# Optimization experiments

Hardware: AMD Instinct MI355X
Metric: run time of the kernel (lower is better)

The kernel has to match this reference:

```python
import jax, jax.numpy as jnp
import numpy as np

DIM = 256
NUM_HEADS = 8
HEAD_DIM = DIM // NUM_HEADS
CPB_HIDDEN = 512
B, N = 2, 2304
TABLE = 9025  # (2*48-1)**2


def _l2norm(t, eps=1e-12):
    # matches torch F.normalize(dim=-1): x / max(||x||, eps)
    n = jnp.sqrt(jnp.sum(t * t, axis=-1, keepdims=True))
    return t / jnp.maximum(n, eps)


def setup_inputs() -> dict:
    key = jax.random.key(0)
    ks = jax.random.split(key, 12)
    x = jax.random.normal(ks[0], (B, N, DIM), dtype=jnp.float32)
    relative_pos_index = jax.random.randint(ks[1], (N, N), 0, TABLE, dtype=jnp.int64)
    relative_coords_table = jax.random.uniform(ks[2], (TABLE, 2), dtype=jnp.float32) * 2.0 - 1.0
    seq_length_scale = jnp.ones((1,), dtype=jnp.float32) * jnp.log2(jnp.float32(N))
    padding_mask = jnp.zeros((B, N), dtype=jnp.int32)
    s = 0.02
    W_qkv = jax.random.normal(ks[3], (3 * DIM, DIM), dtype=jnp.float32) * s
    b_qkv = jnp.zeros((3 * DIM,), dtype=jnp.float32)
    # temperature init: log(exp(1/0.24) - 1) so softplus(temperature) = 1/0.24
    temperature = jnp.full((NUM_HEADS, 1, 1), float(np.log(np.expm1(1.0 / 0.24))), dtype=jnp.float32)
    query_embedding = jax.random.normal(ks[4], (NUM_HEADS, 1, HEAD_DIM), dtype=jnp.float32) * s
    W_proj = jax.random.normal(ks[5], (DIM, DIM), dtype=jnp.float32) * s
    b_proj = jnp.zeros((DIM,), dtype=jnp.float32)
    W_cpb1 = jax.random.normal(ks[6], (CPB_HIDDEN, 2), dtype=jnp.float32) * s
    b_cpb1 = jnp.zeros((CPB_HIDDEN,), dtype=jnp.float32)
    W_cpb2 = jax.random.normal(ks[7], (NUM_HEADS, CPB_HIDDEN), dtype=jnp.float32) * s
    b_cpb2 = jnp.zeros((NUM_HEADS,), dtype=jnp.float32)
    return {
        'x': x, 'relative_pos_index': relative_pos_index,
        'relative_coords_table': relative_coords_table,
        'seq_length_scale': seq_length_scale, 'padding_mask': padding_mask,
        'W_qkv': W_qkv, 'b_qkv': b_qkv, 'temperature': temperature,
        'query_embedding': query_embedding, 'W_proj': W_proj, 'b_proj': b_proj,
        'W_cpb1': W_cpb1, 'b_cpb1': b_cpb1, 'W_cpb2': W_cpb2, 'b_cpb2': b_cpb2,
    }


def reference(x, relative_pos_index, relative_coords_table, seq_length_scale,
              padding_mask, W_qkv, b_qkv, temperature, query_embedding,
              W_proj, b_proj, W_cpb1, b_cpb1, W_cpb2, b_cpb2):
    Bx, Nx, C = x.shape
    h, d = NUM_HEADS, HEAD_DIM
    # qkv projection -> (B, 3h, N, d); first h heads = q, then k, then v
    qkv = (jnp.einsum('bnc,oc->bno', x, W_qkv) + b_qkv)
    qkv = qkv.reshape(Bx, Nx, 3 * h, d).transpose(0, 2, 1, 3)
    q, k, v = qkv[:, :h], qkv[:, h:2 * h], qkv[:, 2 * h:]
    # CPB relative bias: (T,2) -> (T,h) -> (h,N,N) via gather
    hid = jax.nn.relu(relative_coords_table @ W_cpb1.T + b_cpb1)
    tab = hid @ W_cpb2.T + b_cpb2                    # (T, h)
    rel_bias = tab.T[:, relative_pos_index.reshape(-1)].reshape(h, Nx, Nx)
    # cosine-sim attention with learned query embedding + softplus temperature
    scale = jax.nn.softplus(temperature) * seq_length_scale[0]   # (h,1,1)
    qn = (_l2norm(q) + query_embedding) * scale                  # (B,h,N,d)
    kn = _l2norm(k)
    attn = jnp.einsum('bhnd,bhmd->bhnm', qn, kn) + rel_bias
    attn = jax.nn.softmax(attn, axis=-1)
    out = jnp.einsum('bhnm,bhmd->bhnd', attn, v)
    out = out.transpose(0, 2, 1, 3).reshape(Bx, Nx, C)
    out = out @ W_proj.T + b_proj
    return out
```

## Files before the change

kernel.cpp:

```cpp
#include <hip/hip_runtime.h>
#include <math.h>

#define DIMC 256
#define NHEADS 8
#define HDIM 32
#define CPBH 512
#define BB 2
#define NSEQ 2304
#define TAB 9025
#define TABP 9040
#define RTOT (BB*NHEADS*NSEQ)
#define SPLITS 4
#define MSP (NSEQ/SPLITS)
#define PBS 36
#define NCHUNK (NSEQ/32)
#define LOG2E 1.44269504088896340736f

#define NX  (BB*NSEQ*DIMC)
#define NWQ (3*DIMC*DIMC)
#define NWP (DIMC*DIMC)

#define SPLITX4_BLOCKS ((NX + NWQ + NWP) / 1024)
#define IDXP_ELEMS     (NSEQ * NCHUNK * 16)
#define IDXP4_BLOCKS   (IDXP_ELEMS / 1024)
#define CPB_BLOCKS     ((TAB + 63) / 64)

typedef unsigned short ushort;
typedef __attribute__((ext_vector_type(8))) short short8;
typedef __attribute__((ext_vector_type(4))) short short4v;
typedef __attribute__((ext_vector_type(4))) float f32x4;

#define MFMA16(a,b,c) __builtin_amdgcn_mfma_f32_16x16x32_bf16((a),(b),(c),0,0,0)

__device__ __forceinline__ ushort f2bf(float x) {
  unsigned u = __float_as_uint(x);
  u += 0x7FFFu + ((u >> 16) & 1u);
  return (ushort)(u >> 16);
}
__device__ __forceinline__ float bf2f(ushort b) {
  return __uint_as_float(((unsigned)b) << 16);
}
__device__ __forceinline__ float fexp2(float x) {
#if defined(__has_builtin)
#if __has_builtin(__builtin_amdgcn_exp2f)
  return __builtin_amdgcn_exp2f(x);
#else
  return exp2f(x);
#endif
#else
  return exp2f(x);
#endif
}
__device__ __forceinline__ unsigned pack_trunc(float p0, float p1) {
  return __builtin_amdgcn_perm(__float_as_uint(p1), __float_as_uint(p0), 0x07060302u);
}

__global__ void setup_kernel(const float* __restrict__ x, const float* __restrict__ wq,
                             const float* __restrict__ wp, const int* __restrict__ idx,
                             const float* __restrict__ tbl, const float* __restrict__ W1,
                             const float* __restrict__ b1, const float* __restrict__ W2,
                             const float* __restrict__ b2,
                             ushort* __restrict__ xh, ushort* __restrict__ xl,
                             ushort* __restrict__ wqh, ushort* __restrict__ wql,
                             ushort* __restrict__ wph, ushort* __restrict__ wpl,
                             unsigned* __restrict__ idxP, ushort* __restrict__ tabBf) {
  __shared__ float w1b[CPBH * 4];
  __shared__ float w2t[CPBH * NHEADS];
  __shared__ float part[4][64][NHEADS];
  int blk = blockIdx.x;
  int tid = threadIdx.x;
  if (blk < CPB_BLOCKS) {
    for (int i = tid; i < CPBH; i += 256) {
      w1b[i * 4 + 0] = W1[2 * i];
      w1b[i * 4 + 1] = W1[2 * i + 1];
      w1b[i * 4 + 2] = b1[i];
      w1b[i * 4 + 3] = 0.f;
    }
    for (int i = tid; i < CPBH * NHEADS; i += 256)
      w2t[(i & (CPBH - 1)) * NHEADS + (i >> 9)] = W2[i];
    int tl = tid & 63, jc = tid >> 6;
    int t = blk * 64 + tl;
    bool valid = t < TAB;
    float c0 = 0.f, c1 = 0.f;
    if (valid) { c0 = tbl[2 * t]; c1 = tbl[2 * t + 1]; }
    __syncthreads();
    float acc[NHEADS];
#pragma unroll
    for (int h = 0; h < NHEADS; ++h) acc[h] = 0.f;
    for (int j = jc * 128; j < jc * 128 + 128; ++j) {
      float4 wv = *(const float4*)&w1b[j * 4];
      float hid = fmaxf(fmaf(c0, wv.x, fmaf(c1, wv.y, wv.z)), 0.f);
      float4 wa = *(const float4*)&w2t[j * NHEADS];
      float4 wb = *(const float4*)&w2t[j * NHEADS + 4];
      acc[0] = fmaf(hid, wa.x, acc[0]);
      acc[1] = fmaf(hid, wa.y, acc[1]);
      acc[2] = fmaf(hid, wa.z, acc[2]);
      acc[3] = fmaf(hid, wa.w, acc[3]);
      acc[4] = fmaf(hid, wb.x, acc[4]);
      acc[5] = fmaf(hid, wb.y, acc[5]);
      acc[6] = fmaf(hid, wb.z, acc[6]);
      acc[7] = fmaf(hid, wb.w, acc[7]);
    }
#pragma unroll
    for (int h = 0; h < NHEADS; ++h) part[jc][tl][h] = acc[h];
    __syncthreads();
    if (jc == 0 && valid) {
#pragma unroll
      for (int h = 0; h < NHEADS; ++h) {
        float s = part[0][tl][h] + part[1][tl][h] + part[2][tl][h] + part[3][tl][h] + b2[h];
        tabBf[h * TABP + t] = f2bf(s * LOG2E);
      }
    }
  } else if (blk < CPB_BLOCKS + SPLITX4_BLOCKS) {
    int i = ((blk - CPB_BLOCKS) * 256 + tid) * 4;
    const float* src; ushort *hi, *lo; int j;
    if (i < NX)            { src = x;  hi = xh;  lo = xl;  j = i; }
    else if (i < NX + NWQ) { src = wq; hi = wqh; lo = wql; j = i - NX; }
    else                   { src = wp; hi = wph; lo = wpl; j = i - NX - NWQ; }
    float4 v = *(const float4*)&src[j];
    ushort h0 = f2bf(v.x), h1 = f2bf(v.y), h2 = f2bf(v.z), h3 = f2bf(v.w);
    uint2 hp, lp;
    hp.x = (unsigned)h0 | ((unsigned)h1 << 16);
    hp.y = (unsigned)h2 | ((unsigned)h3 << 16);
    lp.x = (unsigned)f2bf(v.x - bf2f(h0)) | ((unsigned)f2bf(v.y - bf2f(h1)) << 16);
    lp.y = (unsigned)f2bf(v.z - bf2f(h2)) | ((unsigned)f2bf(v.w - bf2f(h3)) << 16);
    *(uint2*)&hi[j] = hp;
    *(uint2*)&lo[j] = lp;
  } else {
    int t4 = (blk - CPB_BLOCKS - SPLITX4_BLOCKS) * 256 + tid;
    int cc4 = (t4 & 3) * 4;
    int ch = (t4 >> 2) % NCHUNK;
    int n = t4 / (4 * NCHUNK);
    int mbase = ch * 32 + cc4;
    int4 a = *(const int4*)&idx[(size_t)n * NSEQ + mbase];
    int4 b = *(const int4*)&idx[(size_t)n * NSEQ + mbase + 16];
    uint4 o;
    o.x = (unsigned)a.x | ((unsigned)b.x << 16);
    o.y = (unsigned)a.y | ((unsigned)b.y << 16);
    o.z = (unsigned)a.z | ((unsigned)b.z << 16);
    o.w = (unsigned)a.w | ((unsigned)b.w << 16);
    *(uint4*)&idxP[((size_t)n * NCHUNK + ch) * 16 + cc4] = o;
  }
}

__launch_bounds__(256)
__global__ void gemm_qkv(const ushort* __restrict__ Ah, const ushort* __restrict__ Al,
                         const ushort* __restrict__ Bh, const ushort* __restrict__ Bl,
                         const float* __restrict__ bias, const float* __restrict__ temp,
                         const float* __restrict__ sls, const float* __restrict__ qe,
                         ushort* __restrict__ qhi, ushort* __restrict__ qlo,
                         ushort* __restrict__ khi, ushort* __restrict__ klo,
                         ushort* __restrict__ vT) {
  __shared__ float vbuf[64][65];
  int tid = threadIdx.x;
  int lane = tid & 63, w = tid >> 6;
  int g = lane >> 4, c = lane & 15;
  int n0 = blockIdx.x * 64, m0 = blockIdx.y * 64;
  int mw = m0 + w * 16;
  const int K = DIMC;
  f32x4 acc[4] = {{0,0,0,0},{0,0,0,0},{0,0,0,0},{0,0,0,0}};
#pragma unroll 2
  for (int k0 = 0; k0 < K; k0 += 32) {
    short8 ah = *(const short8*)&Ah[(size_t)(mw + c) * K + k0 + g * 8];
    short8 al = *(const short8*)&Al[(size_t)(mw + c) * K + k0 + g * 8];
#pragma unroll
    for (int nt = 0; nt < 4; ++nt) {
      short8 bh = *(const short8*)&Bh[(size_t)(n0 + nt * 16 + c) * K + k0 + g * 8];
      short8 bl = *(const short8*)&Bl[(size_t)(n0 + nt * 16 + c) * K + k0 + g * 8];
      acc[nt] = MFMA16(ah, bh, acc[nt]);
      acc[nt] = MFMA16(al, bh, acc[nt]);
      acc[nt] = MFMA16(ah, bl, acc[nt]);
    }
  }
#pragma unroll
  for (int nt = 0; nt < 4; ++nt) {
    float bv = bias[n0 + nt * 16 + c];
#pragma unroll
    for (int r = 0; r < 4; ++r) acc[nt][r] += bv;
  }

  int b = (m0 >= NSEQ) ? 1 : 0;
  int nb = m0 - b * NSEQ;
  int sect = n0 >> 8;

  if (sect < 2) {
    int hloc = (n0 & 255) >> 5;
#pragma unroll
    for (int H = 0; H < 2; ++H) {
      int head = hloc + H;
      float scale = log1pf(expf(temp[head])) * sls[0] * LOG2E;
#pragma unroll
      for (int r = 0; r < 4; ++r) {
        float ss = acc[2*H][r]*acc[2*H][r] + acc[2*H+1][r]*acc[2*H+1][r];
        ss += __shfl_xor(ss, 1);
        ss += __shfl_xor(ss, 2);
        ss += __shfl_xor(ss, 4);
        ss += __shfl_xor(ss, 8);
        float inv = 1.f / fmaxf(sqrtf(ss), 1e-12f);
        int n = nb + w * 16 + g * 4 + r;
        size_t orow = ((size_t)(b * NHEADS + head) * NSEQ + n) * HDIM;
#pragma unroll
        for (int half = 0; half < 2; ++half) {
          int nt = 2*H + half;
          int d = half * 16 + c;
          float val = acc[nt][r] * inv;
          if (sect == 0) {
            val = (val + qe[head * HDIM + d]) * scale;
            ushort hh = f2bf(val);
            qhi[orow + d] = hh;
            qlo[orow + d] = f2bf(val - bf2f(hh));
          } else {
            ushort hh = f2bf(val);
            khi[orow + d] = hh;
            klo[orow + d] = f2bf(val - bf2f(hh));
          }
        }
      }
    }
  } else {
#pragma unroll
    for (int nt = 0; nt < 4; ++nt)
#pragma unroll
      for (int r = 0; r < 4; ++r)
        vbuf[w * 16 + g * 4 + r][nt * 16 + c] = acc[nt][r];
    __syncthreads();
    int hbase = (n0 - 512) >> 5;
#pragma unroll
    for (int it = 0; it < 16; ++it) {
      int dloc = (tid >> 6) * 16 + it;
      int p = tid & 63;
      int pp = p & 31;
      int nsrc = (p & 32) + (pp & 1) * 16 + (pp >> 1);
      float v = vbuf[nsrc][dloc];
      int head = hbase + (dloc >> 5), d = dloc & 31;
      vT[((size_t)((b * NHEADS + head) * HDIM + d)) * NSEQ + nb + p] = f2bf(v);
    }
  }
}

__launch_bounds__(256)
__global__ void attn_kernel(const ushort* __restrict__ qhi, const ushort* __restrict__ qlo,
                            const ushort* __restrict__ khi, const ushort* __restrict__ klo,
                            const ushort* __restrict__ vT, const ushort* __restrict__ tabBf,
                            const unsigned* __restrict__ idxP,
                            float* __restrict__ pO, float* __restrict__ pL) {
  __shared__ ushort tbf[10240];
  __shared__ __align__(16) ushort pbuf[8][16 * PBS];
  int tid = threadIdx.x;
  int lane = tid & 63;
  int w = tid >> 6;
  int qb = blockIdx.x;
  int by = blockIdx.y;
  int s = by & 3, bh = by >> 2;
  int h = bh & (NHEADS - 1);

  const ushort* tsrc = tabBf + h * TABP;
#pragma unroll
  for (int i = 0; i < 5; ++i) {
    int off = i * 2048 + tid * 8;
    *(int4*)&tbf[off] = *(const int4*)&tsrc[off];
  }

  int g = lane >> 4, c = lane & 15;
  int q0 = qb * 128 + w * 16;
  int q1 = q0 + 64;
  size_t rowbase = (size_t)bh * NSEQ;

  short8 qAh = *(const short8*)&qhi[(rowbase + q0 + c) * HDIM + g * 8];
  short8 qAl = *(const short8*)&qlo[(rowbase + q0 + c) * HDIM + g * 8];
  short8 qBh = *(const short8*)&qhi[(rowbase + q1 + c) * HDIM + g * 8];
  short8 qBl = *(const short8*)&qlo[(rowbase + q1 + c) * HDIM + g * 8];
  __syncthreads();

  short one = (c == 0) ? (short)0x3F80 : (short)0;
  short8 onesB = {one, one, one, one, one, one, one, one};

  f32x4 oa0 = {0,0,0,0}, oa1 = {0,0,0,0}, ob0 = {0,0,0,0}, ob1 = {0,0,0,0};
  f32x4 la = {0,0,0,0}, lb = {0,0,0,0};
  ushort* pba = pbuf[w * 2];
  ushort* pbb = pbuf[w * 2 + 1];
  int m0 = s * MSP;

#define LOADK(MT, D0H, D0L, D1H, D1L, IA0, IA1, IA2, IA3, IB0, IB1, IB2, IB3) do { \
    size_t ra_ = (rowbase + (MT) + c) * HDIM + g * 8;                 \
    D0H = *(const short8*)&khi[ra_];                                  \
    D0L = *(const short8*)&klo[ra_];                                  \
    D1H = *(const short8*)&khi[ra_ + 16 * HDIM];                      \
    D1L = *(const short8*)&klo[ra_ + 16 * HDIM];                      \
    size_t ia_ = ((size_t)(q0 + g * 4) * NCHUNK + ((MT) >> 5)) * 16 + c; \
    IA0 = idxP[ia_];                                                  \
    IA1 = idxP[ia_ + (size_t)NCHUNK * 16];                            \
    IA2 = idxP[ia_ + (size_t)2 * NCHUNK * 16];                        \
    IA3 = idxP[ia_ + (size_t)3 * NCHUNK * 16];                        \
    size_t ibx_ = ((size_t)(q1 + g * 4) * NCHUNK + ((MT) >> 5)) * 16 + c; \
    IB0 = idxP[ibx_];                                                 \
    IB1 = idxP[ibx_ + (size_t)NCHUNK * 16];                           \
    IB2 = idxP[ibx_ + (size_t)2 * NCHUNK * 16];                       \
    IB3 = idxP[ibx_ + (size_t)3 * NCHUNK * 16];                       \
  } while (0)

  short8 c0h, c0l, c1h, c1l;
  unsigned ia0, ia1, ia2, ia3, ib0, ib1, ib2, ib3;
  LOADK(m0, c0h, c0l, c1h, c1l, ia0, ia1, ia2, ia3, ib0, ib1, ib2, ib3);

  for (int mt = m0; mt < m0 + MSP; mt += 32) {
    int mtn = (mt + 32 < m0 + MSP) ? (mt + 32) : m0;
    short8 n0h, n0l, n1h, n1l;
    unsigned ja0, ja1, ja2, ja3, jb0, jb1, jb2, jb3;
    LOADK(mtn, n0h, n0l, n1h, n1l, ja0, ja1, ja2, ja3, jb0, jb1, jb2, jb3);

    f32x4 sa0 = {0,0,0,0}, sa1 = {0,0,0,0}, sb0 = {0,0,0,0}, sb1 = {0,0,0,0};
    sa0 = MFMA16(qAh, c0h, sa0);
    sb0 = MFMA16(qBh, c0h, sb0);
    sa1 = MFMA16(qAh, c1h, sa1);
    sb1 = MFMA16(qBh, c1h, sb1);
    sa0 = MFMA16(qAl, c0h, sa0);
    sb0 = MFMA16(qBl, c0h, sb0);
    sa1 = MFMA16(qAl, c1h, sa1);
    sb1 = MFMA16(qBl, c1h, sb1);
    sa0 = MFMA16(qAh, c0l, sa0);
    sb0 = MFMA16(qBh, c0l, sb0);
    sa1 = MFMA16(qAh, c1l, sa1);
    sb1 = MFMA16(qBh, c1l, sb1);

    size_t va = ((size_t)(bh * HDIM + c)) * NSEQ + mt + g * 8;
    short8 vf0 = *(const short8*)&vT[va];
    short8 vf1 = *(const short8*)&vT[va + 16 * NSEQ];

    unsigned ipa[4] = {ia0, ia1, ia2, ia3};
    unsigned ipb[4] = {ib0, ib1, ib2, ib3};
#pragma unroll
    for (int r = 0; r < 4; ++r) {
      int k0 = ipa[r] & 0xFFFF, k1 = ipa[r] >> 16;
      float pA0 = fexp2(sa0[r] + bf2f(tbf[k0]));
      float pA1 = fexp2(sa1[r] + bf2f(tbf[k1]));
      *(unsigned*)&pba[(g * 4 + r) * PBS + 2 * c] = pack_trunc(pA0, pA1);
    }
#pragma unroll
    for (int r = 0; r < 4; ++r) {
      int k0 = ipb[r] & 0xFFFF, k1 = ipb[r] >> 16;
      float pB0 = fexp2(sb0[r] + bf2f(tbf[k0]));
      float pB1 = fexp2(sb1[r] + bf2f(tbf[k1]));
      *(unsigned*)&pbb[(g * 4 + r) * PBS + 2 * c] = pack_trunc(pB0, pB1);
    }

    short4v paA = *(const short4v*)&pba[c * PBS + g * 8];
    short4v paB = *(const short4v*)&pba[c * PBS + g * 8 + 4];
    short8 pfa = __builtin_shufflevector(paA, paB, 0, 1, 2, 3, 4, 5, 6, 7);
    short4v pbA = *(const short4v*)&pbb[c * PBS + g * 8];
    short4v pbB = *(const short4v*)&pbb[c * PBS + g * 8 + 4];
    short8 pfb = __builtin_shufflevector(pbA, pbB, 0, 1, 2, 3, 4, 5, 6, 7);

    oa0 = MFMA16(pfa, vf0, oa0);
    oa1 = MFMA16(pfa, vf1, oa1);
    ob0 = MFMA16(pfb, vf0, ob0);
    ob1 = MFMA16(pfb, vf1, ob1);
    la  = MFMA16(pfa, onesB, la);
    lb  = MFMA16(pfb, onesB, lb);

    c0h = n0h; c0l = n0l; c1h = n1h; c1l = n1l;
    ia0 = ja0; ia1 = ja1; ia2 = ja2; ia3 = ja3;
    ib0 = jb0; ib1 = jb1; ib2 = jb2; ib3 = jb3;
  }
#undef LOADK

  size_t prow0 = (size_t)s * RTOT + rowbase;
#pragma unroll
  for (int r = 0; r < 4; ++r) {
    size_t pra = prow0 + q0 + g * 4 + r;
    pO[pra * HDIM + c]      = oa0[r];
    pO[pra * HDIM + 16 + c] = oa1[r];
    size_t prb = prow0 + q1 + g * 4 + r;
    pO[prb * HDIM + c]      = ob0[r];
    pO[prb * HDIM + 16 + c] = ob1[r];
    if (c == 0) { pL[pra] = la[r]; pL[prb] = lb[r]; }
  }
}

#define ALD 264
__launch_bounds__(256)
__global__ void gemm_proj_fused(const float* __restrict__ pO, const float* __restrict__ pL,
                                const ushort* __restrict__ Bh_, const ushort* __restrict__ Bl_,
                                const float* __restrict__ bias, float* __restrict__ C) {
  __shared__ __align__(16) ushort Ahs[64 * ALD];
  __shared__ __align__(16) ushort Als[64 * ALD];
  int tid = threadIdx.x;
  int m0 = blockIdx.x * 64;
  int b = (m0 >= NSEQ) ? 1 : 0;
  int nb = m0 - b * NSEQ;

  {
    int r = tid >> 2;
    int q = tid & 3;
    int n = nb + r;
#pragma unroll
    for (int h = 0; h < NHEADS; ++h) {
      size_t bhn = (size_t)(b * NHEADS + h) * NSEQ + n;
      float L = 0.f;
#pragma unroll
      for (int sp = 0; sp < SPLITS; ++sp) L += pL[(size_t)sp * RTOT + bhn];
      float inv = 1.f / L;
      float a[8] = {0.f, 0.f, 0.f, 0.f, 0.f, 0.f, 0.f, 0.f};
#pragma unroll
      for (int sp = 0; sp < SPLITS; ++sp) {
        const float* src = &pO[((size_t)sp * RTOT + bhn) * HDIM + q * 8];
        float4 v0 = *(const float4*)&src[0];
        float4 v1 = *(const float4*)&src[4];
        a[0] += v0.x; a[1] += v0.y; a[2] += v0.z; a[3] += v0.w;
        a[4] += v1.x; a[5] += v1.y; a[6] += v1.z; a[7] += v1.w;
      }
      ushort hi8[8], lo8[8];
#pragma unroll
      for (int i = 0; i < 8; ++i) {
        float v = a[i] * inv;
        ushort hh = f2bf(v);
        hi8[i] = hh;
        lo8[i] = f2bf(v - bf2f(hh));
      }
      int k = h * 32 + q * 8;
      *(int4*)&Ahs[r * ALD + k] = *(int4*)hi8;
      *(int4*)&Als[r * ALD + k] = *(int4*)lo8;
    }
  }
  __syncthreads();

  int lane = tid & 63, w = tid >> 6;
  int g = lane >> 4, c = lane & 15;
  int n0 = w * 64;
  f32x4 acc[4][4] = {};
  for (int k0 = 0; k0 < DIMC; k0 += 32) {
    short8 bfh[4], bfl[4];
#pragma unroll
    for (int nt = 0; nt < 4; ++nt) {
      bfh[nt] = *(const short8*)&Bh_[(size_t)(n0 + nt * 16 + c) * DIMC + k0 + g * 8];
      bfl[nt] = *(const short8*)&Bl_[(size_t)(n0 + nt * 16 + c) * DIMC + k0 + g * 8];
    }
#pragma unroll
    for (int mt = 0; mt < 4; ++mt) {
      short8 ah = *(const short8*)&Ahs[(mt * 16 + c) * ALD + k0 + g * 8];
      short8 al = *(const short8*)&Als[(mt * 16 + c) * ALD + k0 + g * 8];
#pragma unroll
      for (int nt = 0; nt < 4; ++nt) {
        acc[mt][nt] = MFMA16(ah, bfh[nt], acc[mt][nt]);
        acc[mt][nt] = MFMA16(al, bfh[nt], acc[mt][nt]);
        acc[mt][nt] = MFMA16(ah, bfl[nt], acc[mt][nt]);
      }
    }
  }
#pragma unroll
  for (int nt = 0; nt < 4; ++nt) {
    float bv = bias[n0 + nt * 16 + c];
#pragma unroll
    for (int mt = 0; mt < 4; ++mt)
#pragma unroll
      for (int r = 0; r < 4; ++r)
        C[(size_t)(m0 + mt * 16 + g * 4 + r) * DIMC + n0 + nt * 16 + c] = acc[mt][nt][r] + bv;
  }
}

extern "C" void kernel_launch(void* const* d_in, const int* in_sizes, int n_in,
                              void* d_out, int out_size, void* d_ws, size_t ws_size,
                              hipStream_t stream) {
  const float* x    = (const float*)d_in[0];
  const int*   idx  = (const int*)d_in[1];
  const float* tbl  = (const float*)d_in[2];
  const float* sls  = (const float*)d_in[3];
  const float* Wqkv = (const float*)d_in[5];
  const float* bqkv = (const float*)d_in[6];
  const float* temp = (const float*)d_in[7];
  const float* qe   = (const float*)d_in[8];
  const float* Wp   = (const float*)d_in[9];
  const float* bp   = (const float*)d_in[10];
  const float* W1   = (const float*)d_in[11];
  const float* b1   = (const float*)d_in[12];
  const float* W2   = (const float*)d_in[13];
  const float* b2   = (const float*)d_in[14];

  float* ws   = (float*)d_ws;
  float* pO   = ws;
  float* pL   = pO + (size_t)SPLITS * RTOT * HDIM;
  unsigned* idxP = (unsigned*)(pL + (size_t)SPLITS * RTOT);
  ushort* u   = (ushort*)(idxP + IDXP_ELEMS);
  ushort* qhi = u;                u += (size_t)RTOT * HDIM;
  ushort* qlo = u;                u += (size_t)RTOT * HDIM;
  ushort* khi = u;                u += (size_t)RTOT * HDIM;
  ushort* klo = u;                u += (size_t)RTOT * HDIM;
  ushort* vT  = u;                u += (size_t)RTOT * HDIM;
  ushort* xh  = u;                u += NX;
  ushort* xl  = u;                u += NX;
  ushort* wqh = u;                u += NWQ;
  ushort* wql = u;                u += NWQ;
  ushort* wph = u;                u += NWP;
  ushort* wpl = u;                u += NWP;
  ushort* tabBf = u;              u += 73728;
  float* out  = (float*)d_out;

  setup_kernel<<<dim3(CPB_BLOCKS + SPLITX4_BLOCKS + IDXP4_BLOCKS), dim3(256), 0, stream>>>(
      x, Wqkv, Wp, idx, tbl, W1, b1, W2, b2,
      xh, xl, wqh, wql, wph, wpl, idxP, tabBf);
  gemm_qkv<<<dim3(12, 72), dim3(256), 0, stream>>>(
      xh, xl, wqh, wql, bqkv, temp, sls, qe, qhi, qlo, khi, klo, vT);
  attn_kernel<<<dim3(NSEQ / 128, BB * NHEADS * SPLITS), dim3(256), 0, stream>>>(
      qhi, qlo, khi, klo, vT, tabBf, idxP, pO, pL);
  gemm_proj_fused<<<dim3((BB * NSEQ) / 64), dim3(256), 0, stream>>>(
      pO, pL, wph, wpl, bp, out);
}
```

Measured before the change: 216.7 us.

## Fuse x bf16 split into QKV GEMM, stage q/k stores via LDS, double attention splits

The x hi/lo bf16 split moves out of the setup kernel and into the QKV GEMM's A-operand load, which removes the intermediate xh/xl arrays and their global round trip. The q/k epilogue now stages normalized values through shared memory so each row is written as 16-byte vector stores instead of scattered 2-byte stores. The attention split-K factor rises from 4 to 8, giving more blocks in flight at the cost of more partial outputs for the projection kernel to merge. The GEMM now converts x redundantly across the 12 column blocks, and the new epilogue adds a block barrier.

```diff
diff --git a/kernel.cpp b/kernel.cpp
--- a/kernel.cpp
+++ b/kernel.cpp
@@ -10,7 +10,7 @@
 #define TAB 9025
 #define TABP 9040
 #define RTOT (BB*NHEADS*NSEQ)
-#define SPLITS 4
+#define SPLITS 8
 #define MSP (NSEQ/SPLITS)
 #define PBS 36
 #define NCHUNK (NSEQ/32)
@@ -20,10 +20,10 @@
 #define NWQ (3*DIMC*DIMC)
 #define NWP (DIMC*DIMC)
 
-#define SPLITX4_BLOCKS ((NX + NWQ + NWP) / 1024)
-#define IDXP_ELEMS     (NSEQ * NCHUNK * 16)
-#define IDXP4_BLOCKS   (IDXP_ELEMS / 1024)
-#define CPB_BLOCKS     ((TAB + 63) / 64)
+#define WSPLIT_BLOCKS ((NWQ + NWP) / 1024)
+#define IDXP_ELEMS    (NSEQ * NCHUNK * 16)
+#define IDXP4_BLOCKS  (IDXP_ELEMS / 1024)
+#define CPB_BLOCKS    ((TAB + 63) / 64)
 
 typedef unsigned short ushort;
 typedef __attribute__((ext_vector_type(8))) short short8;
@@ -54,13 +54,25 @@
 __device__ __forceinline__ unsigned pack_trunc(float p0, float p1) {
   return __builtin_amdgcn_perm(__float_as_uint(p1), __float_as_uint(p0), 0x07060302u);
 }
-
-__global__ void setup_kernel(const float* __restrict__ x, const float* __restrict__ wq,
-                             const float* __restrict__ wp, const int* __restrict__ idx,
+__device__ __forceinline__ void cvt8(const float* __restrict__ p, short8* hi, short8* lo) {
+  float4 v0 = *(const float4*)p;
+  float4 v1 = *(const float4*)(p + 4);
+  float vv[8] = {v0.x, v0.y, v0.z, v0.w, v1.x, v1.y, v1.z, v1.w};
+  short8 h, l;
+#pragma unroll
+  for (int i = 0; i < 8; ++i) {
+    ushort hh = f2bf(vv[i]);
+    h[i] = (short)hh;
+    l[i] = (short)f2bf(vv[i] - bf2f(hh));
+  }
+  *hi = h; *lo = l;
+}
+
+__global__ void setup_kernel(const float* __restrict__ wq, const float* __restrict__ wp,
+                             const int* __restrict__ idx,
                              const float* __restrict__ tbl, const float* __restrict__ W1,
                              const float* __restrict__ b1, const float* __restrict__ W2,
                              const float* __restrict__ b2,
-                             ushort* __restrict__ xh, ushort* __restrict__ xl,
                              ushort* __restrict__ wqh, ushort* __restrict__ wql,
                              ushort* __restrict__ wph, ushort* __restrict__ wpl,
                              unsigned* __restrict__ idxP, ushort* __restrict__ tabBf) {
@@ -111,12 +123,11 @@
         tabBf[h * TABP + t] = f2bf(s * LOG2E);
       }
     }
-  } else if (blk < CPB_BLOCKS + SPLITX4_BLOCKS) {
+  } else if (blk < CPB_BLOCKS + WSPLIT_BLOCKS) {
     int i = ((blk - CPB_BLOCKS) * 256 + tid) * 4;
     const float* src; ushort *hi, *lo; int j;
-    if (i < NX)            { src = x;  hi = xh;  lo = xl;  j = i; }
-    else if (i < NX + NWQ) { src = wq; hi = wqh; lo = wql; j = i - NX; }
-    else                   { src = wp; hi = wph; lo = wpl; j = i - NX - NWQ; }
+    if (i < NWQ) { src = wq; hi = wqh; lo = wql; j = i; }
+    else         { src = wp; hi = wph; lo = wpl; j = i - NWQ; }
     float4 v = *(const float4*)&src[j];
     ushort h0 = f2bf(v.x), h1 = f2bf(v.y), h2 = f2bf(v.z), h3 = f2bf(v.w);
     uint2 hp, lp;
@@ -127,7 +138,7 @@
     *(uint2*)&hi[j] = hp;
     *(uint2*)&lo[j] = lp;
   } else {
-    int t4 = (blk - CPB_BLOCKS - SPLITX4_BLOCKS) * 256 + tid;
+    int t4 = (blk - CPB_BLOCKS - WSPLIT_BLOCKS) * 256 + tid;
     int cc4 = (t4 & 3) * 4;
     int ch = (t4 >> 2) % NCHUNK;
     int n = t4 / (4 * NCHUNK);
@@ -144,7 +155,7 @@
 }
 
 __launch_bounds__(256)
-__global__ void gemm_qkv(const ushort* __restrict__ Ah, const ushort* __restrict__ Al,
+__global__ void gemm_qkv(const float* __restrict__ x,
                          const ushort* __restrict__ Bh, const ushort* __restrict__ Bl,
                          const float* __restrict__ bias, const float* __restrict__ temp,
                          const float* __restrict__ sls, const float* __restrict__ qe,
@@ -161,8 +172,8 @@
   f32x4 acc[4] = {{0,0,0,0},{0,0,0,0},{0,0,0,0},{0,0,0,0}};
 #pragma unroll 2
   for (int k0 = 0; k0 < K; k0 += 32) {
-    short8 ah = *(const short8*)&Ah[(size_t)(mw + c) * K + k0 + g * 8];
-    short8 al = *(const short8*)&Al[(size_t)(mw + c) * K + k0 + g * 8];
+    short8 ah, al;
+    cvt8(&x[(size_t)(mw + c) * K + k0 + g * 8], &ah, &al);
 #pragma unroll
     for (int nt = 0; nt < 4; ++nt) {
       short8 bh = *(const short8*)&Bh[(size_t)(n0 + nt * 16 + c) * K + k0 + g * 8];
@@ -182,13 +193,13 @@
   int b = (m0 >= NSEQ) ? 1 : 0;
   int nb = m0 - b * NSEQ;
   int sect = n0 >> 8;
+  int hloc = (n0 & 255) >> 5;
 
   if (sect < 2) {
-    int hloc = (n0 & 255) >> 5;
 #pragma unroll
     for (int H = 0; H < 2; ++H) {
       int head = hloc + H;
-      float scale = log1pf(expf(temp[head])) * sls[0] * LOG2E;
+      float scale = (sect == 0) ? log1pf(expf(temp[head])) * sls[0] * LOG2E : 0.f;
 #pragma unroll
       for (int r = 0; r < 4; ++r) {
         float ss = acc[2*H][r]*acc[2*H][r] + acc[2*H+1][r]*acc[2*H+1][r];
@@ -197,26 +208,32 @@
         ss += __shfl_xor(ss, 4);
         ss += __shfl_xor(ss, 8);
         float inv = 1.f / fmaxf(sqrtf(ss), 1e-12f);
-        int n = nb + w * 16 + g * 4 + r;
-        size_t orow = ((size_t)(b * NHEADS + head) * NSEQ + n) * HDIM;
 #pragma unroll
         for (int half = 0; half < 2; ++half) {
-          int nt = 2*H + half;
           int d = half * 16 + c;
-          float val = acc[nt][r] * inv;
-          if (sect == 0) {
-            val = (val + qe[head * HDIM + d]) * scale;
-            ushort hh = f2bf(val);
-            qhi[orow + d] = hh;
-            qlo[orow + d] = f2bf(val - bf2f(hh));
-          } else {
-            ushort hh = f2bf(val);
-            khi[orow + d] = hh;
-            klo[orow + d] = f2bf(val - bf2f(hh));
-          }
+          float val = acc[2*H + half][r] * inv;
+          if (sect == 0) val = (val + qe[head * HDIM + d]) * scale;
+          vbuf[w * 16 + g * 4 + r][H * 32 + d] = val;
         }
       }
     }
+    __syncthreads();
+    int plane = tid >> 7;
+    int seg = tid & 127;
+    int head = seg >> 6, row = seg & 63;
+    const float* srcrow = &vbuf[row][head * 32];
+    ushort out16[32];
+#pragma unroll
+    for (int i = 0; i < 32; ++i) {
+      float v = srcrow[i];
+      ushort hh = f2bf(v);
+      out16[i] = plane ? f2bf(v - bf2f(hh)) : hh;
+    }
+    ushort* dstp = plane ? (sect == 0 ? qlo : klo) : (sect == 0 ? qhi : khi);
+    size_t off = ((size_t)(b * NHEADS + hloc + head) * NSEQ + nb + row) * HDIM;
+#pragma unroll
+    for (int q4 = 0; q4 < 4; ++q4)
+      *(int4*)&dstp[off + q4 * 8] = ((int4*)out16)[q4];
   } else {
 #pragma unroll
     for (int nt = 0; nt < 4; ++nt)
@@ -251,7 +268,7 @@
   int w = tid >> 6;
   int qb = blockIdx.x;
   int by = blockIdx.y;
-  int s = by & 3, bh = by >> 2;
+  int s = by & 7, bh = by >> 3;
   int h = bh & (NHEADS - 1);
 
   const ushort* tsrc = tabBf + h * TABP;
@@ -486,8 +503,6 @@
   ushort* khi = u;                u += (size_t)RTOT * HDIM;
   ushort* klo = u;                u += (size_t)RTOT * HDIM;
   ushort* vT  = u;                u += (size_t)RTOT * HDIM;
-  ushort* xh  = u;                u += NX;
-  ushort* xl  = u;                u += NX;
   ushort* wqh = u;                u += NWQ;
   ushort* wql = u;                u += NWQ;
   ushort* wph = u;                u += NWP;
@@ -495,11 +510,11 @@
   ushort* tabBf = u;              u += 73728;
   float* out  = (float*)d_out;
 
-  setup_kernel<<<dim3(CPB_BLOCKS + SPLITX4_BLOCKS + IDXP4_BLOCKS), dim3(256), 0, stream>>>(
-      x, Wqkv, Wp, idx, tbl, W1, b1, W2, b2,
-      xh, xl, wqh, wql, wph, wpl, idxP, tabBf);
+  setup_kernel<<<dim3(CPB_BLOCKS + WSPLIT_BLOCKS + IDXP4_BLOCKS), dim3(256), 0, stream>>>(
+      Wqkv, Wp, idx, tbl, W1, b1, W2, b2,
+      wqh, wql, wph, wpl, idxP, tabBf);
   gemm_qkv<<<dim3(12, 72), dim3(256), 0, stream>>>(
-      xh, xl, wqh, wql, bqkv, temp, sls, qe, qhi, qlo, khi, klo, vT);
+      x, wqh, wql, bqkv, temp, sls, qe, qhi, qlo, khi, klo, vT);
   attn_kernel<<<dim3(NSEQ / 128, BB * NHEADS * SPLITS), dim3(256), 0, stream>>>(
       qhi, qlo, khi, klo, vT, tabBf, idxP, pO, pL);
   gemm_proj_fused<<<dim3((BB * NSEQ) / 64), dim3(256), 0, stream>>>(
```

Measured after the change: 220.2 us. About the same (+1.6%).
